# Performance work log

Measured on AMD Instinct MI355X. Metric: run time of the kernel, lower is better.

Reference implementation:

```python
import jax, jax.numpy as jnp
import numpy as np
import math

B, LQ, LK, D, H = 4, 1024, 1024, 1024, 16
DK = D // H
SCALE = 1.0 / math.sqrt(DK)
NEG_INF = -1.0e9


def setup_inputs() -> dict:
    key = jax.random.key(0)
    ks = jax.random.split(key, 18)
    w = lambda k: (jax.random.normal(k, (D, D), dtype=jnp.float32) * 0.02)
    b = lambda k: (jax.random.normal(k, (D,), dtype=jnp.float32) * 0.02)
    mask = jax.random.randint(ks[4], (B, 1, LK), 0, 2).astype(jnp.int32)
    mask = mask.at[..., 0].set(1)  # ensure at least one valid key per row
    return {
        "query": jax.random.normal(ks[0], (B, LQ, D), dtype=jnp.float32),
        "key": jax.random.normal(ks[1], (B, LK, D), dtype=jnp.float32),
        "value": jax.random.normal(ks[2], (B, LK, D), dtype=jnp.float32),
        "weak_rela": jax.random.normal(ks[3], (B, LK, D), dtype=jnp.float32),
        "mask": mask,
        "Wq": w(ks[5]), "bq": b(ks[6]),
        "Wk": w(ks[7]), "bk": b(ks[8]),
        "Wv": w(ks[9]), "bv": b(ks[10]),
        "Wrk": w(ks[11]), "brk": b(ks[12]),
        "Wrv": w(ks[13]), "brv": b(ks[14]),
        "Wo": w(ks[15]), "bo": b(ks[16]),
    }


def _proj(x, W, bias):
    # x: [B, L, D] -> [B, H, L, DK]; torch Linear: y = x @ W.T + b
    y = x @ W.T + bias
    Bn, L, _ = y.shape
    return y.reshape(Bn, L, H, DK).transpose(0, 2, 1, 3)


def reference(query, key, value, weak_rela, mask,
              Wq, bq, Wk, bk, Wv, bv, Wrk, brk, Wrv, brv, Wo, bo):
    q = _proj(query, Wq, bq)        # [B,H,LQ,DK]
    k = _proj(key, Wk, bk)          # [B,H,LK,DK]
    v = _proj(value, Wv, bv)        # [B,H,LK,DK]
    rk = _proj(weak_rela, Wrk, brk) # [B,H,LK,DK]
    rv = _proj(weak_rela, Wrv, brv) # [B,H,LK,DK]

    qk = jnp.einsum('bhqd,bhkd->bhqk', q, k) * SCALE
    qr = jnp.einsum('bhqd,bhkd->bhqk', q, rk) * SCALE

    m = (mask[:, None, :, :] == 0)  # [B,1,1,LK] broadcast over heads/queries
    qk = jnp.where(m, NEG_INF, qk)
    qr = jnp.where(m, NEG_INF, qr)

    p_vis = jax.nn.softmax(qk, axis=-1)
    p_rel = jax.nn.softmax(qr, axis=-1)

    x = (jnp.einsum('bhqk,bhkd->bhqd', p_vis, v)
         + jnp.einsum('bhqk,bhkd->bhqd', p_rel, rv))  # [B,H,LQ,DK]
    x = x.transpose(0, 2, 1, 3).reshape(query.shape[0], -1, H * DK)
    return x @ Wo.T + bo
```

## Files before the change

### kernel.cpp

```cpp
#include <hip/hip_runtime.h>
#include <stdint.h>

#define NB 4
#define NH 16
#define DKH 64
#define DMODEL 1024
#define SEQ 1024
#define SCALE 0.125f
#define NEG_INF -1.0e9f
#define K2E 0.18033688011112042f

typedef __bf16 bf16_t;
typedef __bf16 bf16x8 __attribute__((ext_vector_type(8)));
typedef __bf16 bf16x4v __attribute__((ext_vector_type(4)));
typedef float f32x4 __attribute__((ext_vector_type(4)));
typedef uint32_t u32x4 __attribute__((ext_vector_type(4)));

typedef const uint32_t __attribute__((address_space(1)))* gas_ptr;
typedef uint32_t __attribute__((address_space(3)))* las_ptr;

__device__ __forceinline__ void gload_lds16(const void* g, void* l) {
  __builtin_amdgcn_global_load_lds((gas_ptr)g, (las_ptr)l, 16, 0, 0);
}


__global__ void cvt_multi(const float* __restrict__ i0, const float* __restrict__ i1,
                          const float* __restrict__ i2, const float* __restrict__ i3,
                          const float* __restrict__ i4, const float* __restrict__ i5,
                          bf16_t* o0, bf16_t* o1, bf16_t* o2, bf16_t* o3, bf16_t* o4, bf16_t* o5,
                          int n) {
  const int t = blockIdx.y;
  const float* in = (t == 0) ? i0 : (t == 1) ? i1 : (t == 2) ? i2 : (t == 3) ? i3 : (t == 4) ? i4 : i5;
  bf16_t* out = (t == 0) ? o0 : (t == 1) ? o1 : (t == 2) ? o2 : (t == 3) ? o3 : (t == 4) ? o4 : o5;
  const int idx = (blockIdx.x * 256 + threadIdx.x) * 4;
  if (idx >= n) return;
  const float4 v = *(const float4*)(in + idx);
  bf16x4v p;
  p[0] = (bf16_t)v.x; p[1] = (bf16_t)v.y; p[2] = (bf16_t)v.z; p[3] = (bf16_t)v.w;
  *(bf16x4v*)(out + idx) = p;
}

#define NXE ((size_t)NB * SEQ * DMODEL)
#define NWE ((size_t)DMODEL * DMODEL)

template<int MODE>
__device__ __forceinline__ void gemm128_body(
    const bf16_t* __restrict__ A, const bf16_t* __restrict__ W,
    const float* __restrict__ bias, void* __restrict__ outp,
    int m0, int n0, bf16_t* As, bf16_t* Bs) {
  const int tid = threadIdx.x;
  const int lane = tid & 63;
  const int w = tid >> 6;
  const int wm = w >> 1, wn = w & 1;
  const int g = lane >> 4, c = lane & 15;
  const int lrow = lane >> 3;
  const int lcol = ((lane & 7) * 8) ^ ((lane >> 3) << 3);
  const int sc = (c & 7) << 3;

  f32x4 acc[4][4] = {};

  for (int kt = 0; kt < DMODEL; kt += 64) {
#pragma unroll
    for (int p = 0; p < 4; ++p) {
      const int row = w * 32 + p * 8;
      gload_lds16(A + (size_t)(m0 + row + lrow) * DMODEL + kt + lcol, &As[row * 64]);
      gload_lds16(W + (size_t)(n0 + row + lrow) * DMODEL + kt + lcol, &Bs[row * 64]);
    }
    __syncthreads();
    bf16x8 af[4][2], bfr[4][2];
#pragma unroll
    for (int i = 0; i < 4; ++i)
#pragma unroll
      for (int kk = 0; kk < 2; ++kk) {
        af[i][kk]  = *(const bf16x8*)&As[(wm * 64 + i * 16 + c) * 64 + ((kk * 32 + g * 8) ^ sc)];
        bfr[i][kk] = *(const bf16x8*)&Bs[(wn * 64 + i * 16 + c) * 64 + ((kk * 32 + g * 8) ^ sc)];
      }
#pragma unroll
    for (int i = 0; i < 4; ++i)
#pragma unroll
      for (int j = 0; j < 4; ++j) {
        acc[i][j] = __builtin_amdgcn_mfma_f32_16x16x32_bf16(af[i][0], bfr[j][0], acc[i][j], 0, 0, 0);
        acc[i][j] = __builtin_amdgcn_mfma_f32_16x16x32_bf16(af[i][1], bfr[j][1], acc[i][j], 0, 0, 0);
      }
    __syncthreads();
  }

  float bv4[4];
#pragma unroll
  for (int j = 0; j < 4; ++j) bv4[j] = bias[n0 + wn * 64 + j * 16 + c];

#pragma unroll
  for (int i = 0; i < 4; ++i) {
    const int mrow = m0 + wm * 64 + i * 16 + g * 4;
    const int b_ = mrow >> 10, l_ = mrow & 1023;
#pragma unroll
    for (int j = 0; j < 4; ++j) {
      const int n = n0 + wn * 64 + j * 16 + c;
      if (MODE == 2) {
        float* o = (float*)outp;
#pragma unroll
        for (int r = 0; r < 4; ++r)
          o[(size_t)(mrow + r) * DMODEL + n] = acc[i][j][r] + bv4[j];
      } else if (MODE == 0) {
        bf16_t* o = (bf16_t*)outp;
        const int h_ = n >> 6, dk_ = n & 63;
#pragma unroll
        for (int r = 0; r < 4; ++r)
          o[((size_t)(b_ * NH + h_) * SEQ + l_ + r) * DKH + dk_] =
              (bf16_t)(acc[i][j][r] + bv4[j]);
      } else {
        bf16_t* o = (bf16_t*)outp;
        const int h_ = n >> 6, dk_ = n & 63;
        bf16x4v pk;
#pragma unroll
        for (int r = 0; r < 4; ++r) pk[r] = (bf16_t)(acc[i][j][r] + bv4[j]);
        *(bf16x4v*)&o[((size_t)(b_ * NH + h_) * DKH + dk_) * SEQ + l_] = pk;
      }
    }
  }
}

__global__ void __launch_bounds__(256, 2)
proj_gemm(const bf16_t* __restrict__ Xbase, const bf16_t* __restrict__ Wbase,
          bf16_t* __restrict__ Obase,
          const float* __restrict__ b0, const float* __restrict__ b1,
          const float* __restrict__ b2, const float* __restrict__ b3,
          const float* __restrict__ b4) {
  __shared__ bf16_t As[128 * 64];
  __shared__ bf16_t Bs[128 * 64];
  const int bid = blockIdx.x;
  const int lid = (bid & 7) * 160 + (bid >> 3);
  const int seg = lid >> 8;
  const int rr = lid & 255;
  const int m0 = (rr >> 3) * 128, n0 = (rr & 7) * 128;

  const bf16_t* A = Xbase + (size_t)((seg < 3) ? seg : 3) * NXE;
  const bf16_t* W = Wbase + (size_t)seg * NWE;
  const int ooff = (seg == 0) ? 0 : (seg == 1) ? 1 : (seg == 2) ? 3 : (seg == 3) ? 2 : 4;
  bf16_t* out = Obase + (size_t)ooff * NXE;
  const float* bias = (seg == 0) ? b0 : (seg == 1) ? b1 : (seg == 2) ? b2 : (seg == 3) ? b3 : b4;

  if (seg == 2 || seg == 4) gemm128_body<1>(A, W, bias, out, m0, n0, As, Bs);
  else                      gemm128_body<0>(A, W, bias, out, m0, n0, As, Bs);
}

__global__ void __launch_bounds__(256, 2)
out_gemm(const bf16_t* __restrict__ A, const bf16_t* __restrict__ W,
         const float* __restrict__ bias, float* __restrict__ out) {
  __shared__ bf16_t As[128 * 64];
  __shared__ bf16_t Bs[128 * 64];
  const int bid = blockIdx.x;
  const int lid = (bid & 7) * 32 + (bid >> 3);
  const int m0 = (lid >> 3) * 128, n0 = (lid & 7) * 128;
  gemm128_body<2>(A, W, bias, out, m0, n0, As, Bs);
}

__global__ void __launch_bounds__(256, 2)
attn_kernel(const bf16_t* __restrict__ q, const bf16_t* __restrict__ k,
            const bf16_t* __restrict__ rk, const bf16_t* __restrict__ vT,
            const bf16_t* __restrict__ rvT, const int* __restrict__ mask,
            bf16_t* __restrict__ x) {
  extern __shared__ __align__(256) bf16_t smem[];
  bf16_t* Ks  = smem;
  bf16_t* RKs = Ks  + 64 * 64;
  bf16_t* Vs  = RKs + 64 * 64;
  bf16_t* RVs = Vs  + 64 * 64;
  bf16_t* Pbase = RVs + 64 * 64;
  float* Mb = (float*)(Pbase + 8 * 2048);

  const int tid = threadIdx.x;
  const int lane = tid & 63;
  const int w = tid >> 6;
  const int g = lane >> 4, c = lane & 15;
  const int sc = (c & 7) << 3;
  const int bid = blockIdx.x;
  const int lid = (bid & 7) * 64 + (bid >> 3);
  const int qt = lid & 7;
  const int bh = lid >> 3;
  const int b = bh >> 4, h = bh & 15;
  const int q0 = qt * 128;

  const bf16_t* qp = q + (size_t)bh * SEQ * DKH;
  const bf16_t* kp = k + (size_t)bh * SEQ * DKH;
  const bf16_t* rkp = rk + (size_t)bh * SEQ * DKH;
  const bf16_t* vp = vT + (size_t)bh * DKH * SEQ;
  const bf16_t* rvp = rvT + (size_t)bh * DKH * SEQ;
  const int* mp = mask + b * SEQ;

  const int lrow = lane >> 3;
  const int lcolL = (lane & 7) * 8;
  const int wcol = lcolL ^ (((w * 16 + lrow) & 7) << 3);

  bf16_t* Pwv = Pbase + w * 2048;
  bf16_t* Pwr = Pbase + (4 + w) * 2048;

#pragma unroll
  for (int i = 0; i < 4; ++i) {
    const int idx = i * 256 + tid;
    Mb[idx] = (mp[idx] == 0) ? NEG_INF : 0.0f;
  }

  bf16x8 qf[2][2];
#pragma unroll
  for (int i = 0; i < 2; ++i)
#pragma unroll
    for (int kk = 0; kk < 2; ++kk)
      qf[i][kk] = *(const bf16x8*)(qp + (size_t)(q0 + w * 32 + i * 16 + c) * DKH + kk * 32 + g * 8);

  f32x4 ov[2][4] = {}, orl[2][4] = {};
  float mv[2] = {NEG_INF, NEG_INF}, mr[2] = {NEG_INF, NEG_INF};
  float lv[2] = {0.f, 0.f}, lr[2] = {0.f, 0.f};

  u32x4 st[4][2];

  auto ldreg = [&](int kv0) {
#pragma unroll
    for (int p = 0; p < 2; ++p) {
      const int row = w * 16 + p * 8 + lrow;
      st[0][p] = *(const u32x4*)(kp  + (size_t)(kv0 + row) * DKH + lcolL);
      st[1][p] = *(const u32x4*)(rkp + (size_t)(kv0 + row) * DKH + lcolL);
      st[2][p] = *(const u32x4*)(vp  + (size_t)row * SEQ + kv0 + lcolL);
      st[3][p] = *(const u32x4*)(rvp + (size_t)row * SEQ + kv0 + lcolL);
    }
  };
  auto wrlds = [&]() {
#pragma unroll
    for (int p = 0; p < 2; ++p) {
      const int row = w * 16 + p * 8 + lrow;
      *(u32x4*)&Ks [row * 64 + wcol] = st[0][p];
      *(u32x4*)&RKs[row * 64 + wcol] = st[1][p];
      *(u32x4*)&Vs [row * 64 + wcol] = st[2][p];
      *(u32x4*)&RVs[row * 64 + wcol] = st[3][p];
    }
  };

  auto qk_sm = [&](const bf16_t* Kt, bf16_t* Pb, const f32x4 (&mb)[4],
                   float (&m_s)[2], float (&l_s)[2], f32x4 (&o_s)[2][4]) {
    f32x4 s[2][4];
    {
      bf16x8 kfr[4][2];
#pragma unroll
      for (int f = 0; f < 4; ++f) {
        kfr[f][0] = *(const bf16x8*)&Kt[(f * 16 + c) * 64 + ((g * 8) ^ sc)];
        kfr[f][1] = *(const bf16x8*)&Kt[(f * 16 + c) * 64 + ((32 + g * 8) ^ sc)];
      }
#pragma unroll
      for (int i = 0; i < 2; ++i)
#pragma unroll
        for (int f = 0; f < 4; ++f) {
          f32x4 a = {0.f, 0.f, 0.f, 0.f};
          a = __builtin_amdgcn_mfma_f32_16x16x32_bf16(kfr[f][0], qf[i][0], a, 0, 0, 0);
          a = __builtin_amdgcn_mfma_f32_16x16x32_bf16(kfr[f][1], qf[i][1], a, 0, 0, 0);
          s[i][f] = a;
        }
    }

#pragma unroll
    for (int i = 0; i < 2; ++i)
#pragma unroll
      for (int f = 0; f < 4; ++f)
#pragma unroll
        for (int r = 0; r < 4; ++r)
          s[i][f][r] = s[i][f][r] * K2E + mb[f][r];

#pragma unroll
    for (int i = 0; i < 2; ++i) {
      float tm = fmaxf(fmaxf(s[i][0][0], s[i][0][1]), fmaxf(s[i][0][2], s[i][0][3]));
#pragma unroll
      for (int f = 1; f < 4; ++f)
        tm = fmaxf(tm, fmaxf(fmaxf(s[i][f][0], s[i][f][1]), fmaxf(s[i][f][2], s[i][f][3])));
      tm = fmaxf(tm, __shfl_xor(tm, 16));
      tm = fmaxf(tm, __shfl_xor(tm, 32));
      if (!__all(tm <= m_s[i] + 8.0f)) {
        const float mnew = fmaxf(m_s[i], tm);
        const float sf = __builtin_amdgcn_exp2f(m_s[i] - mnew);
        m_s[i] = mnew;
        l_s[i] *= sf;
#pragma unroll
        for (int jd = 0; jd < 4; ++jd)
#pragma unroll
          for (int r = 0; r < 4; ++r) o_s[i][jd][r] *= sf;
      }
      float pf = 0.f;
#pragma unroll
      for (int f = 0; f < 4; ++f) {
        bf16x4v pk;
#pragma unroll
        for (int r = 0; r < 4; ++r) {
          const float p = __builtin_amdgcn_exp2f(s[i][f][r] - m_s[i]);
          pf += p;
          pk[r] = (bf16_t)p;
        }
        *(bf16x4v*)&Pb[i * 1024 + c * 64 + ((f * 16 + g * 4) ^ sc)] = pk;
      }
      l_s[i] += pf;
    }
  };

  auto pv = [&](const bf16_t* Vt, const bf16_t* Pb, f32x4 (&o_s)[2][4]) {
    bf16x8 pa[2][2];
#pragma unroll
    for (int i = 0; i < 2; ++i) {
      pa[i][0] = *(const bf16x8*)&Pb[i * 1024 + c * 64 + ((g * 8) ^ sc)];
      pa[i][1] = *(const bf16x8*)&Pb[i * 1024 + c * 64 + ((32 + g * 8) ^ sc)];
    }
#pragma unroll
    for (int jd = 0; jd < 4; ++jd) {
      const bf16x8 v0 = *(const bf16x8*)&Vt[(jd * 16 + c) * 64 + ((g * 8) ^ sc)];
      const bf16x8 v1 = *(const bf16x8*)&Vt[(jd * 16 + c) * 64 + ((32 + g * 8) ^ sc)];
#pragma unroll
      for (int i = 0; i < 2; ++i) {
        o_s[i][jd] = __builtin_amdgcn_mfma_f32_16x16x32_bf16(v0, pa[i][0], o_s[i][jd], 0, 0, 0);
        o_s[i][jd] = __builtin_amdgcn_mfma_f32_16x16x32_bf16(v1, pa[i][1], o_s[i][jd], 0, 0, 0);
      }
    }
  };

  ldreg(0);
  wrlds();
  __syncthreads();

  for (int t = 0; t < 16; ++t) {
    const int kv0 = t * 64;

    if (t < 15) ldreg(kv0 + 64);

    f32x4 mb[4];
#pragma unroll
    for (int f = 0; f < 4; ++f)
      mb[f] = *(const f32x4*)&Mb[kv0 + f * 16 + g * 4];

    qk_sm(Ks,  Pwv, mb, mv, lv, ov);
    qk_sm(RKs, Pwr, mb, mr, lr, orl);
    __builtin_amdgcn_s_setprio(1);
    pv(Vs,  Pwv, ov);
    pv(RVs, Pwr, orl);
    __builtin_amdgcn_s_setprio(0);

    if (t < 15) {
      __syncthreads();
      wrlds();
      __syncthreads();
    }
  }

#pragma unroll
  for (int i = 0; i < 2; ++i) {
    lv[i] += __shfl_xor(lv[i], 16); lv[i] += __shfl_xor(lv[i], 32);
    lr[i] += __shfl_xor(lr[i], 16); lr[i] += __shfl_xor(lr[i], 32);
  }

  bf16_t* xb = x + (size_t)b * SEQ * DMODEL + (size_t)h * DKH;
#pragma unroll
  for (int i = 0; i < 2; ++i) {
    const float rlv = 1.0f / lv[i], rlr = 1.0f / lr[i];
    const int qrow = q0 + w * 32 + i * 16 + c;
#pragma unroll
    for (int jd = 0; jd < 4; ++jd) {
      bf16x4v pk;
#pragma unroll
      for (int r = 0; r < 4; ++r)
        pk[r] = (bf16_t)(ov[i][jd][r] * rlv + orl[i][jd][r] * rlr);
      *(bf16x4v*)&xb[(size_t)qrow * DMODEL + jd * 16 + g * 4] = pk;
    }
  }
}

extern "C" void kernel_launch(void* const* d_in, const int* in_sizes, int n_in,
                              void* d_out, int out_size, void* d_ws, size_t ws_size,
                              hipStream_t stream) {
  (void)in_sizes; (void)n_in; (void)out_size; (void)ws_size;
  const float* query = (const float*)d_in[0];
  const float* key_  = (const float*)d_in[1];
  const float* value = (const float*)d_in[2];
  const float* weak  = (const float*)d_in[3];
  const int*   mask  = (const int*)d_in[4];
  const float* Wq  = (const float*)d_in[5];  const float* bq  = (const float*)d_in[6];
  const float* Wk  = (const float*)d_in[7];  const float* bk  = (const float*)d_in[8];
  const float* Wv  = (const float*)d_in[9];  const float* bv  = (const float*)d_in[10];
  const float* Wrk = (const float*)d_in[11]; const float* brk = (const float*)d_in[12];
  const float* Wrv = (const float*)d_in[13]; const float* brv = (const float*)d_in[14];
  const float* Wo  = (const float*)d_in[15]; const float* bo  = (const float*)d_in[16];

  char* ws = (char*)d_ws;
  size_t off = 0;
  auto alloc = [&](size_t bytes) {
    void* p = ws + off;
    off += (bytes + 255) & ~(size_t)255;
    return p;
  };
  const size_t SZ_X = NXE * sizeof(bf16_t);
  const size_t SZ_W = NWE * sizeof(bf16_t);

  bf16_t* Xq = (bf16_t*)alloc(SZ_X);
  bf16_t* Xk = (bf16_t*)alloc(SZ_X);
  bf16_t* Xv = (bf16_t*)alloc(SZ_X);
  bf16_t* Xr = (bf16_t*)alloc(SZ_X);
  bf16_t* Wqb  = (bf16_t*)alloc(SZ_W);
  bf16_t* Wkb  = (bf16_t*)alloc(SZ_W);
  bf16_t* Wvb  = (bf16_t*)alloc(SZ_W);
  bf16_t* Wrkb = (bf16_t*)alloc(SZ_W);
  bf16_t* Wrvb = (bf16_t*)alloc(SZ_W);
  bf16_t* Wob  = (bf16_t*)alloc(SZ_W);
  bf16_t* qh   = (bf16_t*)alloc(SZ_X);
  bf16_t* kh   = (bf16_t*)alloc(SZ_X);
  bf16_t* rkh  = (bf16_t*)alloc(SZ_X);
  bf16_t* vTh  = (bf16_t*)alloc(SZ_X);
  bf16_t* rvTh = (bf16_t*)alloc(SZ_X);
  bf16_t* xh   = (bf16_t*)alloc(SZ_X);
  (void)Xk; (void)Xv; (void)Xr; (void)Wkb; (void)Wvb; (void)Wrkb; (void)Wrvb;
  (void)kh; (void)rkh; (void)vTh; (void)rvTh;

  cvt_multi<<<dim3(4096, 4), 256, 0, stream>>>(query, key_, value, weak, nullptr, nullptr,
                                               Xq, Xk, Xv, Xr, nullptr, nullptr,
                                               NB * SEQ * DMODEL);
  cvt_multi<<<dim3(1024, 6), 256, 0, stream>>>(Wq, Wk, Wv, Wrk, Wrv, Wo,
                                               Wqb, Wkb, Wvb, Wrkb, Wrvb, Wob,
                                               DMODEL * DMODEL);

  proj_gemm<<<dim3(1280), 256, 0, stream>>>(Xq, Wqb, qh, bq, bk, bv, brk, brv);

  attn_kernel<<<dim3(512), 256, 69632, stream>>>(qh, kh, rkh, vTh, rvTh, mask, xh);

  out_gemm<<<dim3(256), 256, 0, stream>>>(xh, Wob, bo, (float*)d_out);
}
```

Measured before the change: 164.5 us.

## Merge conversion launches, shrink output GEMM tile, raise MFMA priority in attention

Folds the two fp32-to-bf16 conversion launches into one grid covering both the activations and the weights, which saves a launch. The weight rows of that grid are mostly idle blocks that exit early. The output projection moves from a 128x128 tile to a dedicated 128x64 tile kernel with a 512-block grid, giving more blocks to fill the CUs on a small GEMM at the cost of more A reloads. The attention QK MFMA section is wrapped in s_setprio to favour matrix-core issue.

```diff
diff --git a/kernel.cpp b/kernel.cpp
--- a/kernel.cpp
+++ b/kernel.cpp
@@ -24,14 +24,29 @@
 }
 
 
-__global__ void cvt_multi(const float* __restrict__ i0, const float* __restrict__ i1,
-                          const float* __restrict__ i2, const float* __restrict__ i3,
-                          const float* __restrict__ i4, const float* __restrict__ i5,
-                          bf16_t* o0, bf16_t* o1, bf16_t* o2, bf16_t* o3, bf16_t* o4, bf16_t* o5,
-                          int n) {
-  const int t = blockIdx.y;
-  const float* in = (t == 0) ? i0 : (t == 1) ? i1 : (t == 2) ? i2 : (t == 3) ? i3 : (t == 4) ? i4 : i5;
-  bf16_t* out = (t == 0) ? o0 : (t == 1) ? o1 : (t == 2) ? o2 : (t == 3) ? o3 : (t == 4) ? o4 : o5;
+#define NXE ((size_t)NB * SEQ * DMODEL)
+#define NWE ((size_t)DMODEL * DMODEL)
+
+__global__ void cvt_all(const float* __restrict__ x0, const float* __restrict__ x1,
+                        const float* __restrict__ x2, const float* __restrict__ x3,
+                        const float* __restrict__ w0, const float* __restrict__ w1,
+                        const float* __restrict__ w2, const float* __restrict__ w3,
+                        const float* __restrict__ w4, const float* __restrict__ w5,
+                        bf16_t* __restrict__ Xbase, bf16_t* __restrict__ Wbase) {
+  const int y = blockIdx.y;
+  const float* in;
+  bf16_t* out;
+  int n;
+  if (y < 4) {
+    in = (y == 0) ? x0 : (y == 1) ? x1 : (y == 2) ? x2 : x3;
+    out = Xbase + (size_t)y * NXE;
+    n = (int)NXE;
+  } else {
+    const int j = y - 4;
+    in = (j == 0) ? w0 : (j == 1) ? w1 : (j == 2) ? w2 : (j == 3) ? w3 : (j == 4) ? w4 : w5;
+    out = Wbase + (size_t)j * NWE;
+    n = (int)NWE;
+  }
   const int idx = (blockIdx.x * 256 + threadIdx.x) * 4;
   if (idx >= n) return;
   const float4 v = *(const float4*)(in + idx);
@@ -39,9 +54,6 @@
   p[0] = (bf16_t)v.x; p[1] = (bf16_t)v.y; p[2] = (bf16_t)v.z; p[3] = (bf16_t)v.w;
   *(bf16x4v*)(out + idx) = p;
 }
-
-#define NXE ((size_t)NB * SEQ * DMODEL)
-#define NWE ((size_t)DMODEL * DMODEL)
 
 template<int MODE>
 __device__ __forceinline__ void gemm128_body(
@@ -96,12 +108,7 @@
 #pragma unroll
     for (int j = 0; j < 4; ++j) {
       const int n = n0 + wn * 64 + j * 16 + c;
-      if (MODE == 2) {
-        float* o = (float*)outp;
-#pragma unroll
-        for (int r = 0; r < 4; ++r)
-          o[(size_t)(mrow + r) * DMODEL + n] = acc[i][j][r] + bv4[j];
-      } else if (MODE == 0) {
+      if (MODE == 0) {
         bf16_t* o = (bf16_t*)outp;
         const int h_ = n >> 6, dk_ = n & 63;
 #pragma unroll
@@ -148,11 +155,69 @@
 out_gemm(const bf16_t* __restrict__ A, const bf16_t* __restrict__ W,
          const float* __restrict__ bias, float* __restrict__ out) {
   __shared__ bf16_t As[128 * 64];
-  __shared__ bf16_t Bs[128 * 64];
+  __shared__ bf16_t Bs[64 * 64];
+  const int tid = threadIdx.x;
+  const int lane = tid & 63;
+  const int w = tid >> 6;
+  const int wm = w >> 1, wn = w & 1;
+  const int g = lane >> 4, c = lane & 15;
   const int bid = blockIdx.x;
-  const int lid = (bid & 7) * 32 + (bid >> 3);
-  const int m0 = (lid >> 3) * 128, n0 = (lid & 7) * 128;
-  gemm128_body<2>(A, W, bias, out, m0, n0, As, Bs);
+  const int lid = (bid & 7) * 64 + (bid >> 3);
+  const int bm = lid >> 4, bn = lid & 15;
+  const int m0 = bm * 128, n0 = bn * 64;
+  const int lrow = lane >> 3;
+  const int lcol = ((lane & 7) * 8) ^ ((lane >> 3) << 3);
+  const int sc = (c & 7) << 3;
+
+  f32x4 acc[4][2] = {};
+
+  for (int kt = 0; kt < DMODEL; kt += 64) {
+#pragma unroll
+    for (int p = 0; p < 4; ++p) {
+      const int row = w * 32 + p * 8;
+      gload_lds16(A + (size_t)(m0 + row + lrow) * DMODEL + kt + lcol, &As[row * 64]);
+    }
+#pragma unroll
+    for (int p = 0; p < 2; ++p) {
+      const int row = w * 16 + p * 8;
+      gload_lds16(W + (size_t)(n0 + row + lrow) * DMODEL + kt + lcol, &Bs[row * 64]);
+    }
+    __syncthreads();
+    bf16x8 af[4][2], bfr[2][2];
+#pragma unroll
+    for (int i = 0; i < 4; ++i)
+#pragma unroll
+      for (int kk = 0; kk < 2; ++kk)
+        af[i][kk] = *(const bf16x8*)&As[(wm * 64 + i * 16 + c) * 64 + ((kk * 32 + g * 8) ^ sc)];
+#pragma unroll
+    for (int j = 0; j < 2; ++j)
+#pragma unroll
+      for (int kk = 0; kk < 2; ++kk)
+        bfr[j][kk] = *(const bf16x8*)&Bs[(wn * 32 + j * 16 + c) * 64 + ((kk * 32 + g * 8) ^ sc)];
+#pragma unroll
+    for (int i = 0; i < 4; ++i)
+#pragma unroll
+      for (int j = 0; j < 2; ++j) {
+        acc[i][j] = __builtin_amdgcn_mfma_f32_16x16x32_bf16(af[i][0], bfr[j][0], acc[i][j], 0, 0, 0);
+        acc[i][j] = __builtin_amdgcn_mfma_f32_16x16x32_bf16(af[i][1], bfr[j][1], acc[i][j], 0, 0, 0);
+      }
+    __syncthreads();
+  }
+
+  float bv2[2];
+#pragma unroll
+  for (int j = 0; j < 2; ++j) bv2[j] = bias[n0 + wn * 32 + j * 16 + c];
+#pragma unroll
+  for (int i = 0; i < 4; ++i) {
+    const int mrow = m0 + wm * 64 + i * 16 + g * 4;
+#pragma unroll
+    for (int j = 0; j < 2; ++j) {
+      const int n = n0 + wn * 32 + j * 16 + c;
+#pragma unroll
+      for (int r = 0; r < 4; ++r)
+        out[(size_t)(mrow + r) * DMODEL + n] = acc[i][j][r] + bv2[j];
+    }
+  }
 }
 
 __global__ void __launch_bounds__(256, 2)
@@ -244,6 +309,7 @@
         kfr[f][0] = *(const bf16x8*)&Kt[(f * 16 + c) * 64 + ((g * 8) ^ sc)];
         kfr[f][1] = *(const bf16x8*)&Kt[(f * 16 + c) * 64 + ((32 + g * 8) ^ sc)];
       }
+      __builtin_amdgcn_s_setprio(1);
 #pragma unroll
       for (int i = 0; i < 2; ++i)
 #pragma unroll
@@ -253,6 +319,7 @@
           a = __builtin_amdgcn_mfma_f32_16x16x32_bf16(kfr[f][1], qf[i][1], a, 0, 0, 0);
           s[i][f] = a;
         }
+      __builtin_amdgcn_s_setprio(0);
     }
 
 #pragma unroll
@@ -411,16 +478,13 @@
   (void)Xk; (void)Xv; (void)Xr; (void)Wkb; (void)Wvb; (void)Wrkb; (void)Wrvb;
   (void)kh; (void)rkh; (void)vTh; (void)rvTh;
 
-  cvt_multi<<<dim3(4096, 4), 256, 0, stream>>>(query, key_, value, weak, nullptr, nullptr,
-                                               Xq, Xk, Xv, Xr, nullptr, nullptr,
-                                               NB * SEQ * DMODEL);
-  cvt_multi<<<dim3(1024, 6), 256, 0, stream>>>(Wq, Wk, Wv, Wrk, Wrv, Wo,
-                                               Wqb, Wkb, Wvb, Wrkb, Wrvb, Wob,
-                                               DMODEL * DMODEL);
+  cvt_all<<<dim3(4096, 10), 256, 0, stream>>>(query, key_, value, weak,
+                                              Wq, Wk, Wv, Wrk, Wrv, Wo,
+                                              Xq, Wqb);
 
   proj_gemm<<<dim3(1280), 256, 0, stream>>>(Xq, Wqb, qh, bq, bk, bv, brk, brv);
 
   attn_kernel<<<dim3(512), 256, 69632, stream>>>(qh, kh, rkh, vTh, rvTh, mask, xh);
 
-  out_gemm<<<dim3(256), 256, 0, stream>>>(xh, Wob, bo, (float*)d_out);
-}
+  out_gemm<<<dim3(512), 256, 0, stream>>>(xh, Wob, bo, (float*)d_out);
+}
```

After: 161.7 us (median of 2 runs). No clear change (-1.7%).
